# Kernel optimization log

Measured on AMD Instinct MI355X. Metric: run time of the kernel, lower is better.

## Reference

```python
import jax, jax.numpy as jnp
import numpy as np
from jax import lax

B, IN_N, MID_N, OUT_N, K, L, WH = 16, 256, 256, 256, 3, 4096, 1024
EPS = 1e-5


def att_conv(x, W, b=None):
    # x: [B, Cin, L], W: [B, Cout, Cin, K] -> per-sample conv1d, padding='same'
    pl, pr = (K - 1) // 2, K // 2
    xp = jnp.pad(x, ((0, 0), (0, 0), (pl, pr)))
    out = 0.
    for t in range(K):  # small fixed K, unrolled shifted-slice einsum
        out = out + jnp.einsum('bcl,boc->bol', lax.dynamic_slice_in_dim(xp, t, L, 2), W[..., t])
    if b is not None:
        out = out + b[:, :, None]
    return out


def batch_norm(x, w, b):
    # training-mode BN over (N, L) per channel, biased variance
    mean = x.mean((0, 2), keepdims=True)
    var = ((x - mean) ** 2).mean((0, 2), keepdims=True)
    return (x - mean) * (w[None, :, None] / jnp.sqrt(var + EPS)) + b[None, :, None]


def se_module(x, w1, b1, w2, b2):
    s = x.mean(2, keepdims=True)  # [B, C, 1]
    s = jax.nn.relu(jnp.einsum('bcl,oc->bol', s, w1) + b1[None, :, None])
    s = jax.nn.sigmoid(jnp.einsum('bcl,oc->bol', s, w2) + b2[None, :, None])
    return x * s


def setup_inputs() -> dict:
    key = jax.random.key(0)
    ks = jax.random.split(key, 16)
    f = lambda k, sh, sc=0.02: jax.random.normal(k, sh, jnp.float32) * sc
    return {
        'x': f(ks[0], (B, IN_N, L), 1.0),
        'att1': f(ks[1], (B, MID_N, WH), 1.0),
        'att2': f(ks[2], (B, MID_N, WH), 1.0),
        'att3': f(ks[3], (B, OUT_N, WH), 1.0),
        'w1_w': f(ks[4], (IN_N * K, WH)), 'w1_b': jnp.zeros((IN_N * K,), jnp.float32),
        'w2_w': f(ks[5], (MID_N * K, WH)), 'w2_b': jnp.zeros((MID_N * K,), jnp.float32),
        'w3_w': f(ks[6], (MID_N * K, WH)), 'w3_b': jnp.zeros((MID_N * K,), jnp.float32),
        'b1_w': f(ks[7], (1, WH)), 'b1_b': jnp.zeros((1,), jnp.float32),
        'bn2_w': jnp.full((MID_N,), 0.1, jnp.float32), 'bn2_b': jnp.zeros((MID_N,), jnp.float32),
        'bn3_w': jnp.full((OUT_N,), 0.1, jnp.float32), 'bn3_b': jnp.zeros((OUT_N,), jnp.float32),
        'se1_w': f(ks[8], (OUT_N, OUT_N)), 'se1_b': jnp.zeros((OUT_N,), jnp.float32),
        'se2_w': f(ks[9], (OUT_N, OUT_N)), 'se2_b': jnp.zeros((OUT_N,), jnp.float32),
    }


def reference(x, att1, att2, att3, w1_w, w1_b, w2_w, w2_b, w3_w, w3_b,
              b1_w, b1_b, bn2_w, bn2_b, bn3_w, bn3_b, se1_w, se1_b, se2_w, se2_b):
    shortcut = x  # in_n == out_n, no downsample -> Identity
    # hypernetwork weight generation (Linear on last dim)
    W1 = (att1 @ w1_w.T + w1_b).reshape(B, MID_N, IN_N, K)
    W2 = (att2 @ w2_w.T + w2_b).reshape(B, MID_N, MID_N, K)
    W3 = (att3 @ w3_w.T + w3_b).reshape(B, OUT_N, MID_N, K)
    b1 = (att1 @ b1_w.T + b1_b)[..., 0]  # [B, mid_n]
    h = jax.nn.relu(att_conv(x, W1, b1))
    h = jax.nn.relu(batch_norm(att_conv(h, W2), bn2_w, bn2_b))
    h = jax.nn.relu(batch_norm(att_conv(h, W3), bn3_w, bn3_b))
    out = jax.nn.relu(se_module(h, se1_w, se1_b, se2_w, se2_b) + shortcut)
    return out
```

## Files before the change

kernel.cpp:

```cpp
#include <hip/hip_runtime.h>
#include <hip/hip_bf16.h>

using bf16 = __hip_bfloat16;
typedef __attribute__((ext_vector_type(4))) float f32x4;
typedef __attribute__((ext_vector_type(8))) short short8;
typedef __attribute__((ext_vector_type(2))) unsigned int uint2v;
typedef __attribute__((ext_vector_type(4))) unsigned int uint4v;

#define DEVI static __device__ __forceinline__

DEVI unsigned short f2b(float f){
  unsigned int u = __float_as_uint(f);
  unsigned int r = (u + 0x7fffu + ((u >> 16) & 1u)) >> 16;
  return (unsigned short)r;
}
DEVI float b2f(unsigned short u){
  return __uint_as_float(((unsigned int)u) << 16);
}

DEVI void gload16(const void* g, void* l){
  __builtin_amdgcn_global_load_lds(
      (const __attribute__((address_space(1))) unsigned int*)g,
      (__attribute__((address_space(3))) unsigned int*)l, 16, 0, 0);
}

__global__ __launch_bounds__(256) void k_transpose_x(const float* __restrict__ x,
                                                     bf16* __restrict__ xt)
{
  __shared__ float tile[64][65];
  const int b = blockIdx.z, l0 = blockIdx.x*64, c0 = blockIdx.y*64;
  const int tid = threadIdx.x;
  {
    const int r = tid >> 2, q = tid & 3;
    const float* src = x + ((size_t)(b*256 + c0 + r))*4096 + l0 + q*16;
    #pragma unroll
    for (int j = 0; j < 4; ++j){
      const f32x4 v = *reinterpret_cast<const f32x4*>(src + j*4);
      #pragma unroll
      for (int e = 0; e < 4; ++e) tile[r][q*16 + j*4 + e] = v[e];
    }
  }
  __syncthreads();
  {
    const int jr = tid >> 2, cq = tid & 3;
    unsigned int w[8];
    #pragma unroll
    for (int e = 0; e < 8; ++e){
      const float lo = tile[cq*16 + 2*e][jr];
      const float hi = tile[cq*16 + 2*e + 1][jr];
      w[e] = (unsigned int)f2b(lo) | ((unsigned int)f2b(hi) << 16);
    }
    unsigned short* dst = (unsigned short*)xt + ((size_t)b*4098 + l0 + jr + 1)*256 + c0 + cq*16;
    uint4v a0 = {w[0],w[1],w[2],w[3]}, a1 = {w[4],w[5],w[6],w[7]};
    *reinterpret_cast<uint4v*>(dst)     = a0;
    *reinterpret_cast<uint4v*>(dst + 8) = a1;
  }
}

__global__ void k_zero_pads(bf16* __restrict__ xt, bf16* __restrict__ h1t)
{
  const int b = blockIdx.x, tid = threadIdx.x;
  const size_t top = (size_t)b*4098*256 + tid;
  const size_t bot = (size_t)b*4098*256 + (size_t)4097*256 + tid;
  unsigned short* px = (unsigned short*)xt;
  unsigned short* ph = (unsigned short*)h1t;
  px[top] = 0; px[bot] = 0; ph[top] = 0; ph[bot] = 0;
}

__global__ __launch_bounds__(256) void k_cvt3(const float* __restrict__ s0, const float* __restrict__ s1,
                                              const float* __restrict__ s2, bf16* __restrict__ dst, int n1)
{
  const size_t total = (size_t)3 * (size_t)n1 / 4;
  for (size_t i = (size_t)blockIdx.x*256 + threadIdx.x; i < total; i += (size_t)gridDim.x*256){
    const size_t e = i*4;
    const int which = (int)(e / (size_t)n1);
    const size_t off = e - (size_t)which*(size_t)n1;
    const float* s = which==0 ? s0 : which==1 ? s1 : s2;
    const f32x4 v = *reinterpret_cast<const f32x4*>(s + off);
    uint2v p;
    p[0] = (unsigned)f2b(v[0]) | ((unsigned)f2b(v[1])<<16);
    p[1] = (unsigned)f2b(v[2]) | ((unsigned)f2b(v[3])<<16);
    *reinterpret_cast<uint2v*>((unsigned short*)dst + e) = p;
  }
}

__global__ __launch_bounds__(256, 3) void k_gen(const float* __restrict__ att1f, const float* __restrict__ att2f,
                                                const float* __restrict__ att3f, const bf16* __restrict__ wbp,
                                                const float* __restrict__ bias0, const float* __restrict__ bias1,
                                                const float* __restrict__ bias2, bf16* __restrict__ Wt)
{
  __shared__ bf16 sAll[24576];
  const int flat = blockIdx.x + blockIdx.z*64;
  const int xcd = flat & 7, s = flat >> 3;
  const int t = s % 3, u = s / 3;
  const int ch = u & 1;
  const int tau = (u >> 1)*8 + xcd;
  const int i = tau >> 5, boc = tau & 31;
  const int bo0 = boc*128, c0 = ch*128;
  const bf16*  __restrict__ A  = wbp + (size_t)i*768*1024 + (size_t)(c0*3 + t)*1024;
  const float* __restrict__ Bf = ((i==0) ? att1f : (i==1) ? att2f : att3f) + (size_t)bo0*1024;
  const float* __restrict__ bias = (i==0) ? bias0 : (i==1) ? bias1 : bias2;
  const int tid = threadIdx.x, lane = tid & 63, wid = tid >> 6;
  const int wr = wid >> 1, wc = wid & 1;
  const int frow = lane & 15, g = lane >> 4;
  f32x4 acc[4][4] = {};

#define GEN_STAGE(kt, bufi) { \
    _Pragma("unroll") \
    for (int j = 0; j < 2; ++j){ \
      const int q = tid + j*256, r = q >> 2, s3 = q & 3; \
      const int cc = (s3 ^ ((r >> 1) & 3)) * 8; \
      gload16(A + (size_t)r*3072 + (kt)*32 + cc, (char*)sAll + (bufi)*8192 + q*16); \
    } \
    _Pragma("unroll") \
    for (int j = 0; j < 4; ++j){ \
      const int q = tid + j*256, r = q >> 3, s7 = q & 7; \
      const int ss = s7 ^ (r & 7); \
      gload16(Bf + (size_t)r*1024 + (kt)*32 + ss*4, (char*)sAll + 16384 + (bufi)*16384 + q*16); \
    } \
  }

  GEN_STAGE(0, 0);
  #pragma unroll 1
  for (int kt = 0; kt < 32; ++kt){
    const int p = kt & 1;
    if (kt + 1 < 32){
      GEN_STAGE(kt+1, p^1);
      asm volatile("s_waitcnt vmcnt(6)" ::: "memory");
    } else {
      asm volatile("s_waitcnt vmcnt(0)" ::: "memory");
    }
    __builtin_amdgcn_s_barrier();
    const char* pA = (const char*)sAll + p*8192;
    const char* pB = (const char*)sAll + 16384 + p*16384;
    short8 bfr[4];
    #pragma unroll
    for (int n = 0; n < 4; ++n){
      const int row = wc*64 + n*16 + frow;
      const f32x4 f0 = *reinterpret_cast<const f32x4*>(pB + row*128 + (((2*g)  ^ (row & 7))*16));
      const f32x4 f1 = *reinterpret_cast<const f32x4*>(pB + row*128 + (((2*g+1)^ (row & 7))*16));
      unsigned int w0, w1, w2, w3;
      asm("v_cvt_pk_bf16_f32 %0, %1, %2" : "=v"(w0) : "v"(f0[0]), "v"(f0[1]));
      asm("v_cvt_pk_bf16_f32 %0, %1, %2" : "=v"(w1) : "v"(f0[2]), "v"(f0[3]));
      asm("v_cvt_pk_bf16_f32 %0, %1, %2" : "=v"(w2) : "v"(f1[0]), "v"(f1[1]));
      asm("v_cvt_pk_bf16_f32 %0, %1, %2" : "=v"(w3) : "v"(f1[2]), "v"(f1[3]));
      union { uint4v u; short8 sv; } cvtu;
      cvtu.u[0] = w0; cvtu.u[1] = w1; cvtu.u[2] = w2; cvtu.u[3] = w3;
      bfr[n] = cvtu.sv;
    }
    __builtin_amdgcn_s_setprio(1);
    #pragma unroll
    for (int m = 0; m < 4; ++m){
      const int row = wr*64 + m*16 + frow;
      const int sl = g ^ ((row >> 1) & 3);
      const short8 af = *reinterpret_cast<const short8*>(pA + row*64 + sl*16);
      #pragma unroll
      for (int n = 0; n < 4; ++n)
        acc[m][n] = __builtin_amdgcn_mfma_f32_16x16x32_bf16(af, bfr[n], acc[m][n], 0, 0, 0);
    }
    __builtin_amdgcn_s_setprio(0);
    __builtin_amdgcn_s_barrier();
  }
#undef GEN_STAGE

  #pragma unroll
  for (int m = 0; m < 4; ++m){
    const int lcol = wr*64 + m*16 + g*4;
    float bi[4];
    #pragma unroll
    for (int j = 0; j < 4; ++j) bi[j] = bias[(c0 + lcol + j)*3 + t];
    #pragma unroll
    for (int n = 0; n < 4; ++n){
      const int row = wc*64 + n*16 + frow;
      uint2v pk;
      pk[0] = (unsigned)f2b(acc[m][n][0] + bi[0]) | ((unsigned)f2b(acc[m][n][1] + bi[1]) << 16);
      pk[1] = (unsigned)f2b(acc[m][n][2] + bi[2]) | ((unsigned)f2b(acc[m][n][3] + bi[3]) << 16);
      const int chunk = (lcol >> 3) ^ (row & 15);
      *reinterpret_cast<uint2v*>((char*)sAll + row*256 + chunk*16 + (g&1)*8) = pk;
    }
  }
  __syncthreads();
  {
    const int bb = boc >> 1, o0 = (boc & 1)*128;
    char* gp = (char*)Wt + 2*(((((size_t)(i*16 + bb)*3 + t)*256 + o0)*256) + c0);
    #pragma unroll
    for (int it = 0; it < 8; ++it){
      const int row = it*16 + (tid >> 4);
      const int c = tid & 15;
      const int cs2 = c ^ (row & 15);
      const uint4v v = *reinterpret_cast<const uint4v*>((const char*)sAll + row*256 + cs2*16);
      *reinterpret_cast<uint4v*>(gp + (size_t)row*512 + c*16) = v;
    }
  }
}

__global__ __launch_bounds__(256) void k_b1(const float* __restrict__ att1, const float* __restrict__ b1w,
                                            const float* __restrict__ b1b, float* __restrict__ out)
{
  const int m = blockIdx.x*4 + (threadIdx.x >> 6);
  const int lane = threadIdx.x & 63;
  const float* a = att1 + (size_t)m*1024;
  float s = 0.f;
  for (int k = lane*4; k < 1024; k += 256){
    const f32x4 v = *reinterpret_cast<const f32x4*>(a + k);
    const f32x4 w = *reinterpret_cast<const f32x4*>(b1w + k);
    s += v[0]*w[0] + v[1]*w[1] + v[2]*w[2] + v[3]*w[3];
  }
  #pragma unroll
  for (int d = 32; d > 0; d >>= 1) s += __shfl_down(s, d);
  if (lane == 0) out[m] = s + b1b[0];
}

__global__ __launch_bounds__(512, 2) void k_conv(const bf16* __restrict__ Xt, const bf16* __restrict__ W,
                                                 const float* __restrict__ bias, bf16* __restrict__ out,
                                                 int outBatchStride, int outRowOff, int applyRelu,
                                                 float* __restrict__ statSum, float* __restrict__ statSq)
{
  __shared__ bf16 sAll[65536];
  const int flat = blockIdx.x + (blockIdx.z << 4);
  const int xcd = flat & 7, sl_ = flat >> 3;
  const int b = 2*xcd + (sl_ >> 4);
  const int l0 = (sl_ & 15) * 256;
  const int tid = threadIdx.x, lane = tid & 63, wid = tid >> 6;
  const int wr = wid >> 2, wc = wid & 3;
  const int frow = lane & 15, g = lane >> 4;
  f32x4 acc[8][4] = {};

  const int r0 = tid >> 3,        cc0 = ((tid & 7) ^ (r0 & 7));
  const int r1 = (tid+512) >> 3,  cc1 = (((tid+512) & 7) ^ (r1 & 7));

#define BARR asm volatile("s_barrier" ::: "memory")

#define STG_A(j, h) { const int t_=(j)%3, c0_=((j)/3)*64; \
    const bf16* gp_ = W + (((size_t)b*3 + t_)*256 + (h)*128)*256 + c0_; \
    char* lb_ = (char*)sAll + (((j)&1)*32768) + (h)*16384; \
    gload16(gp_ + (size_t)r0*256 + cc0*8, lb_ + tid*16); \
    gload16(gp_ + (size_t)r1*256 + cc1*8, lb_ + (tid+512)*16); }

#define STG_B(j, h) { const int t_=(j)%3, c0_=((j)/3)*64; \
    const bf16* gp_ = Xt + ((size_t)b*4098 + l0 + t_ + (h)*128)*256 + c0_; \
    char* lb_ = (char*)sAll + 65536 + (((j)&1)*32768) + (h)*16384; \
    gload16(gp_ + (size_t)r0*256 + cc0*8, lb_ + tid*16); \
    gload16(gp_ + (size_t)r1*256 + cc1*8, lb_ + (tid+512)*16); }

#define RD_A(j, mh) { const char* pa_ = (const char*)sAll + (((j)&1)*32768) + wr*16384; \
    _Pragma("unroll") \
    for (int mf = 0; mf < 4; ++mf){ const int rowl = ((mh)*4 + mf)*16 + frow; \
      _Pragma("unroll") \
      for (int ks = 0; ks < 2; ++ks) \
        afr[mf][ks] = *reinterpret_cast<const short8*>(pa_ + rowl*128 + (((ks*4+g) ^ (rowl & 7))*16)); } }

#define RD_B(j) { const char* pb_ = (const char*)sAll + 65536 + (((j)&1)*32768) + (wc>>1)*16384; \
    _Pragma("unroll") \
    for (int nf = 0; nf < 4; ++nf){ const int rowl = (wc&1)*64 + nf*16 + frow; \
      _Pragma("unroll") \
      for (int ks = 0; ks < 2; ++ks) \
        bfr[nf][ks] = *reinterpret_cast<const short8*>(pb_ + rowl*128 + (((ks*4+g) ^ (rowl & 7))*16)); } }

#define MFMA16(mh, ks) { __builtin_amdgcn_s_setprio(1); \
    _Pragma("unroll") \
    for (int mf = 0; mf < 4; ++mf) \
      _Pragma("unroll") \
      for (int nf = 0; nf < 4; ++nf) \
        acc[(mh)*4+mf][nf] = __builtin_amdgcn_mfma_f32_16x16x32_bf16(afr[mf][ks], bfr[nf][ks], acc[(mh)*4+mf][nf], 0, 0, 0); \
    __builtin_amdgcn_s_setprio(0); }

  STG_A(0,0); STG_A(0,1); STG_B(0,0); STG_B(0,1);
  STG_A(1,0); STG_A(1,1); STG_B(1,0); STG_B(1,1);
  asm volatile("s_waitcnt vmcnt(0)" ::: "memory");
  BARR;

  short8 afr[4][2], bfr[4][2];
  #pragma unroll 1
  for (int i = 0; i < 6; ++i){
    const int J0 = 2*i, J1 = 2*i + 1;
    const bool st = (i < 5);
    RD_A(J0, 0); RD_B(J0);
    if (i > 0) STG_A(J1, 1);
    BARR; MFMA16(0, 0); BARR;
    if (st) STG_B(J0+2, 0);
    BARR; MFMA16(0, 1); BARR;
    RD_A(J0, 1);
    if (st) STG_B(J0+2, 1);
    BARR; MFMA16(1, 0); BARR;
    if (st) STG_A(J0+2, 0);
    if (st) { asm volatile("s_waitcnt vmcnt(6)" ::: "memory"); }
    else    { asm volatile("s_waitcnt vmcnt(0)" ::: "memory"); }
    BARR; MFMA16(1, 1); BARR;
    RD_A(J1, 0); RD_B(J1);
    if (st) STG_A(J0+2, 1);
    BARR; MFMA16(0, 0); BARR;
    if (st) STG_B(J1+2, 0);
    BARR; MFMA16(0, 1); BARR;
    RD_A(J1, 1);
    if (st) STG_B(J1+2, 1);
    BARR; MFMA16(1, 0); BARR;
    if (st) STG_A(J1+2, 0);
    if (st) { asm volatile("s_waitcnt vmcnt(6)" ::: "memory"); }
    else    { asm volatile("s_waitcnt vmcnt(0)" ::: "memory"); }
    BARR; MFMA16(1, 1); BARR;
  }
#undef STG_A
#undef STG_B
#undef RD_A
#undef RD_B
#undef MFMA16
#undef BARR

  float cs[8][4] = {{0.f}}, cq[8][4] = {{0.f}};
  #pragma unroll
  for (int m = 0; m < 8; ++m){
    const int col = wr*128 + m*16 + g*4;
    float bi[4] = {0.f, 0.f, 0.f, 0.f};
    if (bias){
      const f32x4 bv = *reinterpret_cast<const f32x4*>(bias + b*256 + col);
      bi[0]=bv[0]; bi[1]=bv[1]; bi[2]=bv[2]; bi[3]=bv[3];
    }
    #pragma unroll
    for (int n = 0; n < 4; ++n){
      const int row = wc*64 + n*16 + frow;
      float v[4];
      #pragma unroll
      for (int j = 0; j < 4; ++j){
        v[j] = acc[m][n][j] + bi[j];
        if (applyRelu) v[j] = fmaxf(v[j], 0.f);
        cs[m][j] += v[j];
        cq[m][j] += v[j]*v[j];
      }
      uint2v p;
      p[0] = (unsigned)f2b(v[0]) | ((unsigned)f2b(v[1]) << 16);
      p[1] = (unsigned)f2b(v[2]) | ((unsigned)f2b(v[3]) << 16);
      const int chunk = (col >> 3) ^ (row & 31);
      *reinterpret_cast<uint2v*>((char*)sAll + row*512 + chunk*16 + (g&1)*8) = p;
    }
  }
  __syncthreads();
  {
    char* gp = (char*)out + 2*((size_t)b*outBatchStride + (size_t)(l0 + outRowOff)*256);
    #pragma unroll
    for (int p2 = 0; p2 < 16; ++p2){
      const int row = p2*16 + (tid >> 5);
      const int c = tid & 31;
      const int cs2 = c ^ (row & 31);
      const uint4v v = *reinterpret_cast<const uint4v*>((const char*)sAll + row*512 + cs2*16);
      *reinterpret_cast<uint4v*>(gp + (size_t)row*512 + c*16) = v;
    }
  }
  if (statSum){
    #pragma unroll
    for (int m = 0; m < 8; ++m)
      #pragma unroll
      for (int j = 0; j < 4; ++j){
        #pragma unroll
        for (int d = 1; d < 16; d <<= 1){
          cs[m][j] += __shfl_xor(cs[m][j], d);
          cq[m][j] += __shfl_xor(cq[m][j], d);
        }
      }
    __syncthreads();
    float* ls = (float*)sAll;
    float* lq = ls + 1024;
    if (frow == 0){
      #pragma unroll
      for (int m = 0; m < 8; ++m)
        #pragma unroll
        for (int j = 0; j < 4; ++j){
          ls[wid*128 + m*16 + g*4 + j] = cs[m][j];
          lq[wid*128 + m*16 + g*4 + j] = cq[m][j];
        }
    }
    __syncthreads();
    if (tid < 256){
      const int o = tid, half = o >> 7, idx = o & 127;
      float s = 0.f, qq = 0.f;
      #pragma unroll
      for (int wv = 0; wv < 4; ++wv){
        s  += ls[(half*4 + wv)*128 + idx];
        qq += lq[(half*4 + wv)*128 + idx];
      }
      atomicAdd(statSum + o, s);
      atomicAdd(statSq  + o, qq);
    }
  }
}

__global__ void k_bnfin(const float* __restrict__ sum, const float* __restrict__ sq,
                        const float* __restrict__ g, const float* __restrict__ bb,
                        float* __restrict__ scale, float* __restrict__ shift)
{
  const int o = threadIdx.x;
  const float inv = 1.f/65536.f;
  const float m = sum[o]*inv;
  const float v = fmaxf(sq[o]*inv - m*m, 0.f);
  const float sc = g[o] / sqrtf(v + 1e-5f);
  scale[o] = sc;
  shift[o] = bb[o] - m*sc;
}

__global__ __launch_bounds__(256) void k_norm2(const bf16* __restrict__ y, const float* __restrict__ scale,
                                               const float* __restrict__ shift, bf16* __restrict__ h)
{
  const int gr = blockIdx.x*8 + (threadIdx.x >> 5);
  const int oc = threadIdx.x & 31;
  const int b = gr / 4098, lp = gr - b*4098;
  unsigned short* dst = (unsigned short*)h + (size_t)gr*256 + oc*8;
  if (lp == 0 || lp == 4097){
    uint4v z = {0u,0u,0u,0u};
    *reinterpret_cast<uint4v*>(dst) = z;
    return;
  }
  const unsigned short* src = (const unsigned short*)y + ((size_t)b*4096 + (lp-1))*256 + oc*8;
  const uint4v in = *reinterpret_cast<const uint4v*>(src);
  const f32x4 sA0 = *reinterpret_cast<const f32x4*>(scale + oc*8);
  const f32x4 sA1 = *reinterpret_cast<const f32x4*>(scale + oc*8 + 4);
  const f32x4 hA0 = *reinterpret_cast<const f32x4*>(shift + oc*8);
  const f32x4 hA1 = *reinterpret_cast<const f32x4*>(shift + oc*8 + 4);
  uint4v ov;
  #pragma unroll
  for (int e = 0; e < 4; ++e){
    const unsigned int w = in[e];
    const float sc0 = (e<2) ? sA0[2*e] : sA1[2*e-4];
    const float sc1 = (e<2) ? sA0[2*e+1] : sA1[2*e-3];
    const float sh0 = (e<2) ? hA0[2*e] : hA1[2*e-4];
    const float sh1 = (e<2) ? hA0[2*e+1] : hA1[2*e-3];
    const float v0 = fmaxf(b2f((unsigned short)(w & 0xffffu))*sc0 + sh0, 0.f);
    const float v1 = fmaxf(b2f((unsigned short)(w >> 16))*sc1 + sh1, 0.f);
    ov[e] = (unsigned)f2b(v0) | ((unsigned)f2b(v1) << 16);
  }
  *reinterpret_cast<uint4v*>(dst) = ov;
}

__global__ __launch_bounds__(256) void k_norm3(bf16* __restrict__ y, const float* __restrict__ scale,
                                               const float* __restrict__ shift, float* __restrict__ s_sum)
{
  __shared__ float red[8][256];
  const int tid = threadIdx.x;
  const int rr = tid >> 5, oc = tid & 31;
  const size_t row = (size_t)blockIdx.x*8 + rr;
  const int b = (int)(row >> 12);
  unsigned short* p = (unsigned short*)y + row*256 + oc*8;
  const uint4v in = *reinterpret_cast<const uint4v*>(p);
  const f32x4 sA0 = *reinterpret_cast<const f32x4*>(scale + oc*8);
  const f32x4 sA1 = *reinterpret_cast<const f32x4*>(scale + oc*8 + 4);
  const f32x4 hA0 = *reinterpret_cast<const f32x4*>(shift + oc*8);
  const f32x4 hA1 = *reinterpret_cast<const f32x4*>(shift + oc*8 + 4);
  uint4v ov;
  float loc[8];
  #pragma unroll
  for (int e = 0; e < 4; ++e){
    const unsigned int w = in[e];
    const float sc0 = (e<2) ? sA0[2*e] : sA1[2*e-4];
    const float sc1 = (e<2) ? sA0[2*e+1] : sA1[2*e-3];
    const float sh0 = (e<2) ? hA0[2*e] : hA1[2*e-4];
    const float sh1 = (e<2) ? hA0[2*e+1] : hA1[2*e-3];
    const float v0 = fmaxf(b2f((unsigned short)(w & 0xffffu))*sc0 + sh0, 0.f);
    const float v1 = fmaxf(b2f((unsigned short)(w >> 16))*sc1 + sh1, 0.f);
    loc[2*e] = v0; loc[2*e+1] = v1;
    ov[e] = (unsigned)f2b(v0) | ((unsigned)f2b(v1) << 16);
  }
  *reinterpret_cast<uint4v*>(p) = ov;
  #pragma unroll
  for (int j = 0; j < 8; ++j) red[rr][oc*8 + j] = loc[j];
  __syncthreads();
  const int o = tid;
  float tot = 0.f;
  #pragma unroll
  for (int r2 = 0; r2 < 8; ++r2) tot += red[r2][o];
  atomicAdd(&s_sum[(size_t)b*256 + o], tot);
}

__global__ __launch_bounds__(256) void k_se(const float* __restrict__ s_sum, const float* __restrict__ w1,
                                            const float* __restrict__ b1, const float* __restrict__ w2,
                                            const float* __restrict__ b2, float* __restrict__ s2)
{
  __shared__ float sv[256];
  __shared__ float t1[256];
  const int b = blockIdx.x, o = threadIdx.x;
  sv[o] = s_sum[(size_t)b*256 + o] * (1.f/4096.f);
  __syncthreads();
  float a = b1[o];
  for (int c = 0; c < 256; ++c) a += w1[(size_t)o*256 + c] * sv[c];
  t1[o] = fmaxf(a, 0.f);
  __syncthreads();
  float a2 = b2[o];
  for (int c = 0; c < 256; ++c) a2 += w2[(size_t)o*256 + c] * t1[c];
  s2[(size_t)b*256 + o] = 1.f / (1.f + expf(-a2));
}

__global__ __launch_bounds__(256) void k_final(const bf16* __restrict__ h3, const float* __restrict__ s2,
                                               const float* __restrict__ x, float* __restrict__ out)
{
  __shared__ float tile[64][65];
  const int b = blockIdx.z, o0 = blockIdx.y*64, l0 = blockIdx.x*64;
  const int tid = threadIdx.x;
  {
    const int r = tid >> 2, q = tid & 3;
    const unsigned short* src = (const unsigned short*)h3 + ((size_t)b*4096 + l0 + r)*256 + o0 + q*16;
    const uint4v a0 = *reinterpret_cast<const uint4v*>(src);
    const uint4v a1 = *reinterpret_cast<const uint4v*>(src + 8);
    #pragma unroll
    for (int e = 0; e < 4; ++e){
      tile[r][q*16 + 2*e]         = b2f((unsigned short)(a0[e] & 0xffffu));
      tile[r][q*16 + 2*e + 1]     = b2f((unsigned short)(a0[e] >> 16));
      tile[r][q*16 + 8 + 2*e]     = b2f((unsigned short)(a1[e] & 0xffffu));
      tile[r][q*16 + 8 + 2*e + 1] = b2f((unsigned short)(a1[e] >> 16));
    }
  }
  __syncthreads();
  {
    const int orow = tid >> 2, q = tid & 3;
    const int o = o0 + orow;
    const float sc = s2[(size_t)b*256 + o];
    const float* xs = x + ((size_t)b*256 + o)*4096 + l0 + q*16;
    float* dst = out + ((size_t)b*256 + o)*4096 + l0 + q*16;
    #pragma unroll
    for (int k = 0; k < 16; k += 4){
      const f32x4 xv = *reinterpret_cast<const f32x4*>(xs + k);
      f32x4 r;
      #pragma unroll
      for (int e = 0; e < 4; ++e)
        r[e] = fmaxf(tile[q*16 + k + e][orow]*sc + xv[e], 0.f);
      *reinterpret_cast<f32x4*>(dst + k) = r;
    }
  }
}

extern "C" void kernel_launch(void* const* d_in, const int* in_sizes, int n_in,
                              void* d_out, int out_size, void* d_ws, size_t ws_size,
                              hipStream_t stream)
{
  const float* x     = (const float*)d_in[0];
  const float* att1  = (const float*)d_in[1];
  const float* att2  = (const float*)d_in[2];
  const float* att3  = (const float*)d_in[3];
  const float* w1_w  = (const float*)d_in[4];
  const float* w1_b  = (const float*)d_in[5];
  const float* w2_w  = (const float*)d_in[6];
  const float* w2_b  = (const float*)d_in[7];
  const float* w3_w  = (const float*)d_in[8];
  const float* w3_b  = (const float*)d_in[9];
  const float* b1_w  = (const float*)d_in[10];
  const float* b1_b  = (const float*)d_in[11];
  const float* bn2_w = (const float*)d_in[12];
  const float* bn2_b = (const float*)d_in[13];
  const float* bn3_w = (const float*)d_in[14];
  const float* bn3_b = (const float*)d_in[15];
  const float* se1_w = (const float*)d_in[16];
  const float* se1_b = (const float*)d_in[17];
  const float* se2_w = (const float*)d_in[18];
  const float* se2_b = (const float*)d_in[19];

  char* ws = (char*)d_ws;
  bf16*  xT   = (bf16*)(ws + 0);
  bf16*  h1T  = (bf16*)(ws + 33570816);
  bf16*  y2T  = (bf16*)(ws + 67141632);
  bf16*  h2T  = (bf16*)(ws + 100696064);
  bf16*  Wt   = (bf16*)(ws + 134266880);
  bf16*  wb   = (bf16*)(ws + 178307072);
  float* b1v  = (float*)(ws + 183025664);
  float* st   = (float*)(ws + 183042048);
  float* bn2sum = st;
  float* bn2sq  = st + 256;
  float* bn3sum = st + 512;
  float* bn3sq  = st + 768;
  float* s_sum  = st + 1024;
  float* scale2 = st + 5120;
  float* shift2 = st + 5376;
  float* scale3 = st + 5632;
  float* shift3 = st + 5888;
  float* s2v    = st + 6144;
  bf16*  y3T  = (bf16*)(ws + 0);

  hipMemsetAsync(st, 0, 5120*sizeof(float), stream);

  k_transpose_x<<<dim3(64,4,16),256,0,stream>>>(x, xT);
  k_zero_pads<<<16,256,0,stream>>>(xT, h1T);
  k_cvt3<<<512,256,0,stream>>>(w1_w, w2_w, w3_w, wb, 768*1024);
  k_gen<<<dim3(64,1,9),256,0,stream>>>(att1, att2, att3, wb, w1_b, w2_b, w3_b, Wt);
  k_b1<<<1024,256,0,stream>>>(att1, b1_w, b1_b, b1v);

  k_conv<<<dim3(16,1,16),512,0,stream>>>(xT,  Wt,                           b1v,     h1T, 4098*256, 1, 1, nullptr, nullptr);
  k_conv<<<dim3(16,1,16),512,0,stream>>>(h1T, Wt + (size_t)1*16*3*256*256,  nullptr, y2T, 4096*256, 0, 0, bn2sum, bn2sq);
  k_bnfin<<<1,256,0,stream>>>(bn2sum, bn2sq, bn2_w, bn2_b, scale2, shift2);
  k_norm2<<<8196,256,0,stream>>>(y2T, scale2, shift2, h2T);
  k_conv<<<dim3(16,1,16),512,0,stream>>>(h2T, Wt + (size_t)2*16*3*256*256,  nullptr, y3T, 4096*256, 0, 0, bn3sum, bn3sq);
  k_bnfin<<<1,256,0,stream>>>(bn3sum, bn3sq, bn3_w, bn3_b, scale3, shift3);
  k_norm3<<<8192,256,0,stream>>>(y3T, scale3, shift3, s_sum);
  k_se<<<16,256,0,stream>>>(s_sum, se1_w, se1_b, se2_w, se2_b, s2v);
  k_final<<<dim3(64,4,16),256,0,stream>>>((const bf16*)y3T, s2v, x, (float*)d_out);
}
```

Baseline: 307.6 us.

## Fuse BN3 normalize into final kernel, reuse bf16 xT, merge conv MFMA phases

The third BN normalize+ReLU is no longer written back to y3 by k_norm3. It becomes k_sum3, which only accumulates the SE channel sums, while k_final recomputes the normalized value from y3 using scale3/shift3. k_final also reads the residual shortcut from the already-transposed bf16 xT instead of the fp32 x, and y3T moves to the h1T slot so xT survives. Separately, the conv main loop pairs MFMA blocks under one setprio region and groups staging loads, which halves the number of barriers. Together these cut a full-size write plus half the shortcut read and reduce synchronisation, at the cost of rounding the residual input to bf16 precision.

```diff
diff --git a/kernel.cpp b/kernel.cpp
--- a/kernel.cpp
+++ b/kernel.cpp
@@ -257,13 +257,12 @@
       for (int ks = 0; ks < 2; ++ks) \
         bfr[nf][ks] = *reinterpret_cast<const short8*>(pb_ + rowl*128 + (((ks*4+g) ^ (rowl & 7))*16)); } }
 
-#define MFMA16(mh, ks) { __builtin_amdgcn_s_setprio(1); \
+#define MFMA16(mh, ks) { \
     _Pragma("unroll") \
     for (int mf = 0; mf < 4; ++mf) \
       _Pragma("unroll") \
       for (int nf = 0; nf < 4; ++nf) \
-        acc[(mh)*4+mf][nf] = __builtin_amdgcn_mfma_f32_16x16x32_bf16(afr[mf][ks], bfr[nf][ks], acc[(mh)*4+mf][nf], 0, 0, 0); \
-    __builtin_amdgcn_s_setprio(0); }
+        acc[(mh)*4+mf][nf] = __builtin_amdgcn_mfma_f32_16x16x32_bf16(afr[mf][ks], bfr[nf][ks], acc[(mh)*4+mf][nf], 0, 0, 0); }
 
   STG_A(0,0); STG_A(0,1); STG_B(0,0); STG_B(0,1);
   STG_A(1,0); STG_A(1,1); STG_B(1,0); STG_B(1,1);
@@ -277,28 +276,35 @@
     const bool st = (i < 5);
     RD_A(J0, 0); RD_B(J0);
     if (i > 0) STG_A(J1, 1);
-    BARR; MFMA16(0, 0); BARR;
     if (st) STG_B(J0+2, 0);
-    BARR; MFMA16(0, 1); BARR;
+    BARR;
+    __builtin_amdgcn_s_setprio(1); MFMA16(0,0); MFMA16(0,1); __builtin_amdgcn_s_setprio(0);
+    BARR;
     RD_A(J0, 1);
-    if (st) STG_B(J0+2, 1);
-    BARR; MFMA16(1, 0); BARR;
-    if (st) STG_A(J0+2, 0);
-    if (st) { asm volatile("s_waitcnt vmcnt(6)" ::: "memory"); }
-    else    { asm volatile("s_waitcnt vmcnt(0)" ::: "memory"); }
-    BARR; MFMA16(1, 1); BARR;
+    if (st){
+      STG_B(J0+2, 1); STG_A(J0+2, 0);
+      asm volatile("s_waitcnt vmcnt(6)" ::: "memory");
+    } else {
+      asm volatile("s_waitcnt vmcnt(0)" ::: "memory");
+    }
+    BARR;
+    __builtin_amdgcn_s_setprio(1); MFMA16(1,0); MFMA16(1,1); __builtin_amdgcn_s_setprio(0);
+    BARR;
     RD_A(J1, 0); RD_B(J1);
-    if (st) STG_A(J0+2, 1);
-    BARR; MFMA16(0, 0); BARR;
-    if (st) STG_B(J1+2, 0);
-    BARR; MFMA16(0, 1); BARR;
+    if (st){ STG_A(J0+2, 1); STG_B(J1+2, 0); }
+    BARR;
+    __builtin_amdgcn_s_setprio(1); MFMA16(0,0); MFMA16(0,1); __builtin_amdgcn_s_setprio(0);
+    BARR;
     RD_A(J1, 1);
-    if (st) STG_B(J1+2, 1);
-    BARR; MFMA16(1, 0); BARR;
-    if (st) STG_A(J1+2, 0);
-    if (st) { asm volatile("s_waitcnt vmcnt(6)" ::: "memory"); }
-    else    { asm volatile("s_waitcnt vmcnt(0)" ::: "memory"); }
-    BARR; MFMA16(1, 1); BARR;
+    if (st){
+      STG_B(J1+2, 1); STG_A(J1+2, 0);
+      asm volatile("s_waitcnt vmcnt(6)" ::: "memory");
+    } else {
+      asm volatile("s_waitcnt vmcnt(0)" ::: "memory");
+    }
+    BARR;
+    __builtin_amdgcn_s_setprio(1); MFMA16(1,0); MFMA16(1,1); __builtin_amdgcn_s_setprio(0);
+    BARR;
   }
 #undef STG_A
 #undef STG_B
@@ -430,21 +436,20 @@
   *reinterpret_cast<uint4v*>(dst) = ov;
 }
 
-__global__ __launch_bounds__(256) void k_norm3(bf16* __restrict__ y, const float* __restrict__ scale,
-                                               const float* __restrict__ shift, float* __restrict__ s_sum)
+__global__ __launch_bounds__(256) void k_sum3(const bf16* __restrict__ y, const float* __restrict__ scale,
+                                              const float* __restrict__ shift, float* __restrict__ s_sum)
 {
   __shared__ float red[8][256];
   const int tid = threadIdx.x;
   const int rr = tid >> 5, oc = tid & 31;
   const size_t row = (size_t)blockIdx.x*8 + rr;
   const int b = (int)(row >> 12);
-  unsigned short* p = (unsigned short*)y + row*256 + oc*8;
+  const unsigned short* p = (const unsigned short*)y + row*256 + oc*8;
   const uint4v in = *reinterpret_cast<const uint4v*>(p);
   const f32x4 sA0 = *reinterpret_cast<const f32x4*>(scale + oc*8);
   const f32x4 sA1 = *reinterpret_cast<const f32x4*>(scale + oc*8 + 4);
   const f32x4 hA0 = *reinterpret_cast<const f32x4*>(shift + oc*8);
   const f32x4 hA1 = *reinterpret_cast<const f32x4*>(shift + oc*8 + 4);
-  uint4v ov;
   float loc[8];
   #pragma unroll
   for (int e = 0; e < 4; ++e){
@@ -453,12 +458,9 @@
     const float sc1 = (e<2) ? sA0[2*e+1] : sA1[2*e-3];
     const float sh0 = (e<2) ? hA0[2*e] : hA1[2*e-4];
     const float sh1 = (e<2) ? hA0[2*e+1] : hA1[2*e-3];
-    const float v0 = fmaxf(b2f((unsigned short)(w & 0xffffu))*sc0 + sh0, 0.f);
-    const float v1 = fmaxf(b2f((unsigned short)(w >> 16))*sc1 + sh1, 0.f);
-    loc[2*e] = v0; loc[2*e+1] = v1;
-    ov[e] = (unsigned)f2b(v0) | ((unsigned)f2b(v1) << 16);
-  }
-  *reinterpret_cast<uint4v*>(p) = ov;
+    loc[2*e]   = fmaxf(b2f((unsigned short)(w & 0xffffu))*sc0 + sh0, 0.f);
+    loc[2*e+1] = fmaxf(b2f((unsigned short)(w >> 16))*sc1 + sh1, 0.f);
+  }
   #pragma unroll
   for (int j = 0; j < 8; ++j) red[rr][oc*8 + j] = loc[j];
   __syncthreads();
@@ -487,39 +489,63 @@
   s2[(size_t)b*256 + o] = 1.f / (1.f + expf(-a2));
 }
 
-__global__ __launch_bounds__(256) void k_final(const bf16* __restrict__ h3, const float* __restrict__ s2,
-                                               const float* __restrict__ x, float* __restrict__ out)
-{
-  __shared__ float tile[64][65];
+__global__ __launch_bounds__(256) void k_final(const bf16* __restrict__ y3, const bf16* __restrict__ xt,
+                                               const float* __restrict__ scale, const float* __restrict__ shift,
+                                               const float* __restrict__ s2, float* __restrict__ out)
+{
+  __shared__ float tH[64][65];
+  __shared__ float tX[64][65];
   const int b = blockIdx.z, o0 = blockIdx.y*64, l0 = blockIdx.x*64;
   const int tid = threadIdx.x;
   {
     const int r = tid >> 2, q = tid & 3;
-    const unsigned short* src = (const unsigned short*)h3 + ((size_t)b*4096 + l0 + r)*256 + o0 + q*16;
-    const uint4v a0 = *reinterpret_cast<const uint4v*>(src);
-    const uint4v a1 = *reinterpret_cast<const uint4v*>(src + 8);
+    const int cb = o0 + q*16;
+    const unsigned short* sy = (const unsigned short*)y3 + ((size_t)b*4096 + l0 + r)*256 + cb;
+    const unsigned short* sx = (const unsigned short*)xt + ((size_t)b*4098 + l0 + r + 1)*256 + cb;
+    const uint4v y0 = *reinterpret_cast<const uint4v*>(sy);
+    const uint4v y1 = *reinterpret_cast<const uint4v*>(sy + 8);
+    const uint4v x0 = *reinterpret_cast<const uint4v*>(sx);
+    const uint4v x1 = *reinterpret_cast<const uint4v*>(sx + 8);
+    const f32x4 sc0 = *reinterpret_cast<const f32x4*>(scale + cb);
+    const f32x4 sc1 = *reinterpret_cast<const f32x4*>(scale + cb + 4);
+    const f32x4 sc2 = *reinterpret_cast<const f32x4*>(scale + cb + 8);
+    const f32x4 sc3 = *reinterpret_cast<const f32x4*>(scale + cb + 12);
+    const f32x4 sh0 = *reinterpret_cast<const f32x4*>(shift + cb);
+    const f32x4 sh1 = *reinterpret_cast<const f32x4*>(shift + cb + 4);
+    const f32x4 sh2 = *reinterpret_cast<const f32x4*>(shift + cb + 8);
+    const f32x4 sh3 = *reinterpret_cast<const f32x4*>(shift + cb + 12);
     #pragma unroll
     for (int e = 0; e < 4; ++e){
-      tile[r][q*16 + 2*e]         = b2f((unsigned short)(a0[e] & 0xffffu));
-      tile[r][q*16 + 2*e + 1]     = b2f((unsigned short)(a0[e] >> 16));
-      tile[r][q*16 + 8 + 2*e]     = b2f((unsigned short)(a1[e] & 0xffffu));
-      tile[r][q*16 + 8 + 2*e + 1] = b2f((unsigned short)(a1[e] >> 16));
+      const float a0 = (e<2) ? sc0[2*e] : sc1[2*e-4];
+      const float a1 = (e<2) ? sc0[2*e+1] : sc1[2*e-3];
+      const float b0 = (e<2) ? sh0[2*e] : sh1[2*e-4];
+      const float b1v = (e<2) ? sh0[2*e+1] : sh1[2*e-3];
+      tH[r][q*16 + 2*e]     = fmaxf(b2f((unsigned short)(y0[e] & 0xffffu))*a0 + b0, 0.f);
+      tH[r][q*16 + 2*e + 1] = fmaxf(b2f((unsigned short)(y0[e] >> 16))*a1 + b1v, 0.f);
+      tX[r][q*16 + 2*e]     = b2f((unsigned short)(x0[e] & 0xffffu));
+      tX[r][q*16 + 2*e + 1] = b2f((unsigned short)(x0[e] >> 16));
+      const float c0v = (e<2) ? sc2[2*e] : sc3[2*e-4];
+      const float c1v = (e<2) ? sc2[2*e+1] : sc3[2*e-3];
+      const float d0 = (e<2) ? sh2[2*e] : sh3[2*e-4];
+      const float d1 = (e<2) ? sh2[2*e+1] : sh3[2*e-3];
+      tH[r][q*16 + 8 + 2*e]     = fmaxf(b2f((unsigned short)(y1[e] & 0xffffu))*c0v + d0, 0.f);
+      tH[r][q*16 + 8 + 2*e + 1] = fmaxf(b2f((unsigned short)(y1[e] >> 16))*c1v + d1, 0.f);
+      tX[r][q*16 + 8 + 2*e]     = b2f((unsigned short)(x1[e] & 0xffffu));
+      tX[r][q*16 + 8 + 2*e + 1] = b2f((unsigned short)(x1[e] >> 16));
     }
   }
   __syncthreads();
   {
     const int orow = tid >> 2, q = tid & 3;
     const int o = o0 + orow;
-    const float sc = s2[(size_t)b*256 + o];
-    const float* xs = x + ((size_t)b*256 + o)*4096 + l0 + q*16;
+    const float sfac = s2[(size_t)b*256 + o];
     float* dst = out + ((size_t)b*256 + o)*4096 + l0 + q*16;
     #pragma unroll
     for (int k = 0; k < 16; k += 4){
-      const f32x4 xv = *reinterpret_cast<const f32x4*>(xs + k);
       f32x4 r;
       #pragma unroll
       for (int e = 0; e < 4; ++e)
-        r[e] = fmaxf(tile[q*16 + k + e][orow]*sc + xv[e], 0.f);
+        r[e] = fmaxf(tH[q*16 + k + e][orow]*sfac + tX[q*16 + k + e][orow], 0.f);
       *reinterpret_cast<f32x4*>(dst + k) = r;
     }
   }
@@ -569,7 +595,7 @@
   float* scale3 = st + 5632;
   float* shift3 = st + 5888;
   float* s2v    = st + 6144;
-  bf16*  y3T  = (bf16*)(ws + 0);
+  bf16*  y3T  = (bf16*)(ws + 33570816);
 
   hipMemsetAsync(st, 0, 5120*sizeof(float), stream);
 
@@ -585,7 +611,7 @@
   k_norm2<<<8196,256,0,stream>>>(y2T, scale2, shift2, h2T);
   k_conv<<<dim3(16,1,16),512,0,stream>>>(h2T, Wt + (size_t)2*16*3*256*256,  nullptr, y3T, 4096*256, 0, 0, bn3sum, bn3sq);
   k_bnfin<<<1,256,0,stream>>>(bn3sum, bn3sq, bn3_w, bn3_b, scale3, shift3);
-  k_norm3<<<8192,256,0,stream>>>(y3T, scale3, shift3, s_sum);
+  k_sum3<<<8192,256,0,stream>>>(y3T, scale3, shift3, s_sum);
   k_se<<<16,256,0,stream>>>(s_sum, se1_w, se1_b, se2_w, se2_b, s2v);
-  k_final<<<dim3(64,4,16),256,0,stream>>>((const bf16*)y3T, s2v, x, (float*)d_out);
-}
+  k_final<<<dim3(64,4,16),256,0,stream>>>(y3T, xT, scale3, shift3, s2v, (float*)d_out);
+}
```

Measured after the change: 298.7 us. 1.03x faster.
